# Kernel tuning notes

Measured on AMD Instinct MI355X. Metric: run time of the kernel, lower is better.

The kernel has to match this reference:

```python
import jax, jax.numpy as jnp
import numpy as np

B, C, IMG, PS, S, D, H, HD, L, OUT = 512, 3, 36, 6, 36, 768, 12, 64, 4, 256

def _pos_embedding(seq_len, dim):
    # NOTE: cos at even indices, sin at odd (as in the torch source)
    position = np.arange(seq_len, dtype=np.float32)[:, None]
    div = np.exp(np.arange(0, dim, 2, dtype=np.float32) * -(np.log(10000.0) / dim))
    emb = np.zeros((seq_len, dim), dtype=np.float32)
    emb[:, 0::2] = np.cos(position * div)
    emb[:, 1::2] = np.sin(position * div)
    return jnp.asarray(emb)

def setup_inputs():
    ks = jax.random.split(jax.random.key(0), 10)
    sc = lambda f: 1.0 / np.sqrt(f)
    return {
        'batch': jax.random.normal(ks[0], (B, C, IMG, IMG), jnp.float32),
        'W_patch': jax.random.normal(ks[1], (D, PS * PS), jnp.float32) * sc(PS * PS),
        'b_patch': jnp.zeros((D,), jnp.float32),
        'pos': _pos_embedding(S, D),
        'ln1_g': jnp.ones((L, D), jnp.float32),
        'ln1_b': jnp.zeros((L, D), jnp.float32),
        'Wq': jax.random.normal(ks[2], (L, H, HD, HD), jnp.float32) * sc(HD),
        'bq': jnp.zeros((L, H, HD), jnp.float32),
        'Wk': jax.random.normal(ks[3], (L, H, HD, HD), jnp.float32) * sc(HD),
        'bk': jnp.zeros((L, H, HD), jnp.float32),
        'Wv': jax.random.normal(ks[4], (L, H, HD, HD), jnp.float32) * sc(HD),
        'bv': jnp.zeros((L, H, HD), jnp.float32),
        'ln2_g': jnp.ones((L, D), jnp.float32),
        'ln2_b': jnp.zeros((L, D), jnp.float32),
        'W1': jax.random.normal(ks[5], (L, 2 * D, D), jnp.float32) * sc(D),
        'b1': jnp.zeros((L, 2 * D), jnp.float32),
        'W2': jax.random.normal(ks[6], (L, D, 2 * D), jnp.float32) * sc(2 * D),
        'b2': jnp.zeros((L, D), jnp.float32),
        'W_out': jax.random.normal(ks[7], (OUT, D), jnp.float32) * sc(D),
        'b_out': jnp.zeros((OUT,), jnp.float32),
    }

def _layernorm(x, g, b):
    m = jnp.mean(x, axis=-1, keepdims=True)
    v = jnp.mean((x - m) ** 2, axis=-1, keepdims=True)
    return (x - m) / jnp.sqrt(v + 1e-5) * g + b

def _forward(batch, W_patch, b_patch, pos, ln1_g, ln1_b, Wq, bq, Wk, bk, Wv, bv,
             ln2_g, ln2_b, W1, b1, W2, b2, W_out, b_out):
    b_, c_ = batch.shape[0], batch.shape[1]
    # patchify: (B,C,36,36) -> (B,C,36 patches,36 pixels), matching torch unfold+reshape
    p = batch.reshape(b_, c_, IMG // PS, PS, IMG // PS, PS)
    p = p.transpose(0, 1, 2, 4, 3, 5).reshape(b_, c_, S, PS * PS)
    z = p @ W_patch.T + b_patch + pos  # pos broadcasts over (B,C)
    scale = 1.0 / np.sqrt(HD)
    for l in range(L):
        # pre-LN then batched per-head attention (collapses the python loops)
        h = _layernorm(z, ln1_g[l], ln1_b[l]).reshape(b_, c_, S, H, HD)
        q = jnp.einsum('bcshd,hed->bcshe', h, Wq[l]) + bq[l]
        k = jnp.einsum('bcshd,hed->bcshe', h, Wk[l]) + bk[l]
        v = jnp.einsum('bcshd,hed->bcshe', h, Wv[l]) + bv[l]
        attn = jax.nn.softmax(jnp.einsum('bcshe,bcthe->bchst', q, k) * scale, axis=-1)
        o = jnp.einsum('bchst,bcthe->bcshe', attn, v).reshape(b_, c_, S, D)
        z = z + o
        z = _layernorm(z, ln2_g[l], ln2_b[l])
        z = z + (jax.nn.relu(z @ W1[l].T + b1[l]) @ W2[l].T + b2[l])
    return z @ W_out.T + b_out

def reference(batch, W_patch, b_patch, pos, ln1_g, ln1_b, Wq, bq, Wk, bk, Wv, bv,
              ln2_g, ln2_b, W1, b1, W2, b2, W_out, b_out):
    return _forward(batch, W_patch, b_patch, pos, ln1_g, ln1_b, Wq, bq, Wk, bk, Wv, bv,
                    ln2_g, ln2_b, W1, b1, W2, b2, W_out, b_out)
```

## Files before the change

### kernel.cpp

```cpp
#include <hip/hip_runtime.h>
#include <hip/hip_bf16.h>
#include <cstdint>
#include <cstddef>

typedef __bf16 bf16;
typedef bf16 bf16x8 __attribute__((ext_vector_type(8)));
typedef bf16 bf16x4 __attribute__((ext_vector_type(4)));
typedef float f32x4 __attribute__((ext_vector_type(4)));
typedef unsigned int u32;

#define GLD_LDS16(gptr, lptr)                                                        \
  __builtin_amdgcn_global_load_lds((const __attribute__((address_space(1))) u32*)(gptr), \
                                   (__attribute__((address_space(3))) u32*)(lptr), 16, 0, 0)

static constexpr int S = 36, D = 768, H = 12, HD = 64, DFF = 1536;
static constexpr int BC = 1536;
static constexpr int M = BC * S;
static constexpr int OUTD = 256;

__global__ __launch_bounds__(256) void f2b_kernel(const float* __restrict__ in,
                                                  bf16* __restrict__ out, int n4) {
  int i = blockIdx.x * 256 + threadIdx.x;
  if (i < n4) {
    float4 f = ((const float4*)in)[i];
    bf16x4 o = {(bf16)f.x, (bf16)f.y, (bf16)f.z, (bf16)f.w};
    ((bf16x4*)out)[i] = o;
  }
}

__global__ __launch_bounds__(256) void zerok(float* __restrict__ p, int n) {
  int i = blockIdx.x * 256 + threadIdx.x;
  if (i < n) p[i] = 0.f;
}
__global__ __launch_bounds__(256) void stats_fin(const float* __restrict__ sacc,
                                                 float* __restrict__ stats, int n) {
  int i = blockIdx.x * 256 + threadIdx.x;
  if (i < n) {
    float sm = sacc[(size_t)i * 2] * (1.f / 768.f);
    float sq = sacc[(size_t)i * 2 + 1] * (1.f / 768.f);
    float var = sq - sm * sm;
    stats[(size_t)i * 2] = sm;
    stats[(size_t)i * 2 + 1] = rsqrtf(var + 1e-5f);
  }
}

__global__ __launch_bounds__(64) void qk_prep(const float* __restrict__ Wq,
                                              const float* __restrict__ Wk,
                                              const float* __restrict__ bq,
                                              bf16* __restrict__ wb,
                                              float* __restrict__ vkout) {
  int lh = blockIdx.x;
  int e = threadIdx.x;
  __shared__ float Wqs[64][64];
  __shared__ float Wks[64][64];
  const float* wqp = Wq + (size_t)lh * 4096;
  const float* wkp = Wk + (size_t)lh * 4096;
  for (int i = e; i < 4096; i += 64) {
    Wqs[i >> 6][i & 63] = wqp[i];
    Wks[i >> 6][i & 63] = wkp[i];
  }
  __syncthreads();
  float ks[64];
#pragma unroll
  for (int f = 0; f < 64; ++f) ks[f] = Wks[f][e];
  for (int d0 = 0; d0 < 64; d0 += 4) {
    float a0 = 0.f, a1 = 0.f, a2 = 0.f, a3 = 0.f;
#pragma unroll
    for (int f = 0; f < 64; ++f) {
      float4 wq4 = *(const float4*)&Wqs[f][d0];
      a0 += wq4.x * ks[f]; a1 += wq4.y * ks[f];
      a2 += wq4.z * ks[f]; a3 += wq4.w * ks[f];
    }
    bf16x4 o = {(bf16)a0, (bf16)a1, (bf16)a2, (bf16)a3};
    *(bf16x4*)&wb[(size_t)lh * 4096 + e * 64 + d0] = o;
  }
  const float* bqp = bq + lh * 64;
  float acc = 0.f;
#pragma unroll
  for (int f = 0; f < 64; ++f) acc += ks[f] * bqp[f];
  vkout[lh * 64 + e] = acc;
}

__global__ __launch_bounds__(256) void patch_embed(const float* __restrict__ batch,
                                                   const float* __restrict__ Wp,
                                                   const float* __restrict__ bp,
                                                   const float* __restrict__ pos,
                                                   float* __restrict__ z) {
  int bc = blockIdx.x, tid = threadIdx.x;
  __shared__ float p[36][40];
  for (int i = tid; i < 1296; i += 256) {
    float f = batch[(size_t)bc * 1296 + i];
    int row = i / 36, col = i - row * 36;
    p[(row / 6) * 6 + col / 6][(row % 6) * 6 + (col % 6)] = f;
  }
  __syncthreads();
  for (int c0 = 0; c0 < 768; c0 += 256) {
    int d = c0 + tid;
    float wr[36];
    const float4* wp4 = (const float4*)(Wp + (size_t)d * 36);
#pragma unroll
    for (int q = 0; q < 9; ++q) {
      float4 f = wp4[q];
      wr[q * 4] = f.x; wr[q * 4 + 1] = f.y; wr[q * 4 + 2] = f.z; wr[q * 4 + 3] = f.w;
    }
    float gb = bp[d];
    for (int s = 0; s < 36; ++s) {
      float acc = 0.f;
#pragma unroll
      for (int k = 0; k < 36; ++k) acc += p[s][k] * wr[k];
      z[((size_t)bc * 36 + s) * 768 + d] = acc + gb + pos[s * 768 + d];
    }
  }
}

__global__ __launch_bounds__(256) void ln_stats(const float* __restrict__ zin,
                                                float* __restrict__ stats) {
  int row = blockIdx.x * 4 + (threadIdx.x >> 6);
  int lane = threadIdx.x & 63;
  const float* zr = zin + (size_t)row * D;
  float x[12];
#pragma unroll
  for (int i = 0; i < 12; ++i) x[i] = zr[i * 64 + lane];
  float s = 0.f;
#pragma unroll
  for (int i = 0; i < 12; ++i) s += x[i];
#pragma unroll
  for (int off = 32; off >= 1; off >>= 1) s += __shfl_xor(s, off, 64);
  float m = s * (1.f / 768.f);
  float v = 0.f;
#pragma unroll
  for (int i = 0; i < 12; ++i) { float dd = x[i] - m; v += dd * dd; }
#pragma unroll
  for (int off = 32; off >= 1; off >>= 1) v += __shfl_xor(v, off, 64);
  v *= (1.f / 768.f);
  if (lane == 0) {
    stats[(size_t)row * 2] = m;
    stats[(size_t)row * 2 + 1] = rsqrtf(v + 1e-5f);
  }
}

__global__ __launch_bounds__(256) void ln_inplace(float* __restrict__ z,
                                                  const float* __restrict__ g,
                                                  const float* __restrict__ bt) {
  int row = blockIdx.x * 4 + (threadIdx.x >> 6);
  int lane = threadIdx.x & 63;
  float* zr = z + (size_t)row * D;
  float x[12];
#pragma unroll
  for (int i = 0; i < 12; ++i) x[i] = zr[i * 64 + lane];
  float s = 0.f;
#pragma unroll
  for (int i = 0; i < 12; ++i) s += x[i];
#pragma unroll
  for (int off = 32; off >= 1; off >>= 1) s += __shfl_xor(s, off, 64);
  float m = s * (1.f / 768.f);
  float v = 0.f;
#pragma unroll
  for (int i = 0; i < 12; ++i) { float dd = x[i] - m; v += dd * dd; }
#pragma unroll
  for (int off = 32; off >= 1; off >>= 1) v += __shfl_xor(v, off, 64);
  v *= (1.f / 768.f);
  float rstd = rsqrtf(v + 1e-5f);
#pragma unroll
  for (int i = 0; i < 12; ++i) {
    int d = i * 64 + lane;
    zr[d] = (x[i] - m) * rstd * g[d] + bt[d];
  }
}

__global__ __launch_bounds__(64) void attn_kernel(const float* __restrict__ zg,
                                                  const float* __restrict__ stats,
                                                  const float* __restrict__ g1,
                                                  const float* __restrict__ b1_,
                                                  const bf16* __restrict__ Wqk,
                                                  const bf16* __restrict__ Wv,
                                                  const float* __restrict__ vk,
                                                  const float* __restrict__ bv,
                                                  float* __restrict__ z) {
  int head = blockIdx.x;
  int bc = blockIdx.y;
  __shared__ __align__(16) bf16 gb[48 * 72];
  __shared__ __align__(16) bf16 vt[64 * 72];
  int lane = threadIdx.x;
  int lr = lane & 15, quad = lane >> 4;

#pragma unroll
  for (int t0 = 0; t0 < 16; ++t0) vt[lane * 72 + 48 + t0] = (bf16)0.f;

  const float* zsrc = zg + ((size_t)bc * S) * D + head * HD;
  const float* st = stats + (size_t)bc * S * 2;

  float gv[2][8], bvv[2][8];
#pragma unroll
  for (int kt = 0; kt < 2; ++kt) {
    int c0 = head * HD + kt * 32 + quad * 8;
    float4 ga = *(const float4*)(g1 + c0);
    float4 gb2 = *(const float4*)(g1 + c0 + 4);
    float4 ba = *(const float4*)(b1_ + c0);
    float4 bb2 = *(const float4*)(b1_ + c0 + 4);
    gv[kt][0] = ga.x; gv[kt][1] = ga.y; gv[kt][2] = ga.z; gv[kt][3] = ga.w;
    gv[kt][4] = gb2.x; gv[kt][5] = gb2.y; gv[kt][6] = gb2.z; gv[kt][7] = gb2.w;
    bvv[kt][0] = ba.x; bvv[kt][1] = ba.y; bvv[kt][2] = ba.z; bvv[kt][3] = ba.w;
    bvv[kt][4] = bb2.x; bvv[kt][5] = bb2.y; bvv[kt][6] = bb2.z; bvv[kt][7] = bb2.w;
  }

  bf16x8 hfrag[3][2];
#pragma unroll
  for (int mt = 0; mt < 3; ++mt) {
    int srow = mt * 16 + lr;
    if (srow < 36) {
      float mm = st[srow * 2], rr = st[srow * 2 + 1];
#pragma unroll
      for (int kt = 0; kt < 2; ++kt) {
        int c0 = kt * 32 + quad * 8;
        float4 f0 = *(const float4*)(zsrc + (size_t)srow * D + c0);
        float4 f1 = *(const float4*)(zsrc + (size_t)srow * D + c0 + 4);
        float hv[8] = {f0.x, f0.y, f0.z, f0.w, f1.x, f1.y, f1.z, f1.w};
        bf16x8 o;
#pragma unroll
        for (int j = 0; j < 8; ++j) o[j] = (bf16)((hv[j] - mm) * rr * gv[kt][j] + bvv[kt][j]);
        hfrag[mt][kt] = o;
      }
    } else {
#pragma unroll
      for (int kt = 0; kt < 2; ++kt) {
        bf16x8 o;
#pragma unroll
        for (int j = 0; j < 8; ++j) o[j] = (bf16)0.f;
        hfrag[mt][kt] = o;
      }
    }
  }

  float vkv[2][8];
#pragma unroll
  for (int kt = 0; kt < 2; ++kt) {
    int c0 = head * 64 + kt * 32 + quad * 8;
    float4 va = *(const float4*)(vk + c0);
    float4 vb2 = *(const float4*)(vk + c0 + 4);
    vkv[kt][0] = va.x; vkv[kt][1] = va.y; vkv[kt][2] = va.z; vkv[kt][3] = va.w;
    vkv[kt][4] = vb2.x; vkv[kt][5] = vb2.y; vkv[kt][6] = vb2.z; vkv[kt][7] = vb2.w;
  }
  float tv[3];
#pragma unroll
  for (int mt = 0; mt < 3; ++mt) {
    float sp = 0.f;
#pragma unroll
    for (int kt = 0; kt < 2; ++kt)
#pragma unroll
      for (int j = 0; j < 8; ++j) sp += (float)hfrag[mt][kt][j] * vkv[kt][j];
    sp += __shfl_xor(sp, 16, 64);
    sp += __shfl_xor(sp, 32, 64);
    tv[mt] = sp;
  }

  const bf16* Wm[2] = {Wqk + (size_t)head * 4096, Wv + (size_t)head * 4096};
  const float* bvp = bv + head * 64;
  for (int p = 0; p < 2; ++p) {
    bf16x8 bfr[4][2];
#pragma unroll
    for (int nt = 0; nt < 4; ++nt)
#pragma unroll
      for (int kt = 0; kt < 2; ++kt)
        bfr[nt][kt] = *(const bf16x8*)(Wm[p] + (nt * 16 + lr) * 64 + kt * 32 + quad * 8);
#pragma unroll
    for (int mt = 0; mt < 3; ++mt) {
      f32x4 acc[4] = {};
#pragma unroll
      for (int kt = 0; kt < 2; ++kt)
#pragma unroll
        for (int nt = 0; nt < 4; ++nt)
          acc[nt] = __builtin_amdgcn_mfma_f32_16x16x32_bf16(hfrag[mt][kt], bfr[nt][kt], acc[nt], 0, 0, 0);
#pragma unroll
      for (int nt = 0; nt < 4; ++nt) {
        float bb = (p == 1) ? bvp[nt * 16 + lr] : 0.f;
#pragma unroll
        for (int r = 0; r < 4; ++r) {
          int s2 = mt * 16 + quad * 4 + r;
          int e = nt * 16 + lr;
          float val = acc[nt][r] + bb;
          if (p == 0) gb[s2 * 72 + e] = (bf16)val;
          else vt[e * 72 + s2] = (bf16)val;
        }
      }
    }
  }
  __syncthreads();

  f32x4 sc[3][3];
#pragma unroll
  for (int mt = 0; mt < 3; ++mt)
#pragma unroll
    for (int nt = 0; nt < 3; ++nt) {
      f32x4 a = {};
#pragma unroll
      for (int kt = 0; kt < 2; ++kt) {
        bf16x8 af = *(const bf16x8*)&gb[(mt * 16 + lr) * 72 + kt * 32 + quad * 8];
        a = __builtin_amdgcn_mfma_f32_16x16x32_bf16(af, hfrag[nt][kt], a, 0, 0, 0);
      }
      int t = nt * 16 + lr;
#pragma unroll
      for (int r = 0; r < 4; ++r) {
        float v = (a[r] + tv[nt]) * 0.125f;
        if (t >= 36) v = -1e30f;
        sc[mt][nt][r] = v;
      }
    }
  __syncthreads();

#pragma unroll
  for (int mt = 0; mt < 3; ++mt) {
    float mx[4], sum[4];
#pragma unroll
    for (int r = 0; r < 4; ++r)
      mx[r] = fmaxf(fmaxf(sc[mt][0][r], sc[mt][1][r]), sc[mt][2][r]);
#pragma unroll
    for (int r = 0; r < 4; ++r)
#pragma unroll
      for (int off = 8; off >= 1; off >>= 1) mx[r] = fmaxf(mx[r], __shfl_xor(mx[r], off, 64));
#pragma unroll
    for (int r = 0; r < 4; ++r) sum[r] = 0.f;
#pragma unroll
    for (int nt = 0; nt < 3; ++nt)
#pragma unroll
      for (int r = 0; r < 4; ++r) {
        float e = __expf(sc[mt][nt][r] - mx[r]);
        sc[mt][nt][r] = e;
        sum[r] += e;
      }
#pragma unroll
    for (int r = 0; r < 4; ++r)
#pragma unroll
      for (int off = 8; off >= 1; off >>= 1) sum[r] += __shfl_xor(sum[r], off, 64);
#pragma unroll
    for (int nt = 0; nt < 4; ++nt)
#pragma unroll
      for (int r = 0; r < 4; ++r) {
        int s2 = mt * 16 + quad * 4 + r;
        int t = nt * 16 + lr;
        float pv = (nt < 3) ? sc[mt][nt][r] / sum[r] : 0.f;
        gb[s2 * 72 + t] = (bf16)pv;
      }
  }
  __syncthreads();

#pragma unroll
  for (int mt = 0; mt < 3; ++mt) {
    f32x4 o[4] = {};
#pragma unroll
    for (int kt = 0; kt < 2; ++kt) {
      bf16x8 a = *(const bf16x8*)&gb[(mt * 16 + lr) * 72 + kt * 32 + quad * 8];
#pragma unroll
      for (int nt = 0; nt < 4; ++nt) {
        bf16x8 b = *(const bf16x8*)&vt[(nt * 16 + lr) * 72 + kt * 32 + quad * 8];
        o[nt] = __builtin_amdgcn_mfma_f32_16x16x32_bf16(a, b, o[nt], 0, 0, 0);
      }
    }
#pragma unroll
    for (int nt = 0; nt < 4; ++nt)
#pragma unroll
      for (int r = 0; r < 4; ++r) {
        int s2 = mt * 16 + quad * 4 + r;
        if (s2 < 36) {
          int e = nt * 16 + lr;
          size_t idx = ((size_t)bc * S + s2) * D + head * HD + e;
          z[idx] += o[nt][r];
        }
      }
  }
}

template <int N, int K, int MODE, int AF32>
__global__ __launch_bounds__(256) void gemm_bt(const void* __restrict__ A,
                                               const bf16* __restrict__ Bw,
                                               const float* __restrict__ bias,
                                               const float* __restrict__ res,
                                               void* __restrict__ outp,
                                               float* __restrict__ sacc) {
  constexpr int BK = 64;
  __shared__ __align__(16) bf16 As[128 * BK];
  __shared__ __align__(16) bf16 Bs[128 * BK];
  int tid = threadIdx.x;
  int bn = blockIdx.x, bm = blockIdx.y;
  if ((gridDim.y & 7) == 0) {
    int gx = gridDim.x, gy = gridDim.y;
    int h = bm * gx + bn;
    int x = h & 7, k = h >> 3;
    int gpc = gy >> 3;
    bm = x * gpc + k / gx;
    bn = k - (k / gx) * gx;
  }
  const bf16* Abf = (const bf16*)A + (size_t)bm * 128 * K;
  const float* Af = (const float*)A + (size_t)bm * 128 * K;
  const bf16* Bb = Bw + (size_t)bn * 128 * K;
  int lane = tid & 63, wave = tid >> 6;
  int wm = (wave >> 1) * 64, wn = (wave & 1) * 64;
  int lr = lane & 15, quad = lane >> 4;
  f32x4 acc[4][4] = {};
  for (int k0 = 0; k0 < K; k0 += BK) {
    if (AF32) {
#pragma unroll
      for (int r = 0; r < 8; ++r) {
        int c = r * 256 + tid;
        int row = c >> 4, col4 = (c & 15) * 4;
        float4 f = *(const float4*)(Af + (size_t)row * K + k0 + col4);
        bf16x4 o = {(bf16)f.x, (bf16)f.y, (bf16)f.z, (bf16)f.w};
        *(bf16x4*)&As[row * BK + col4] = o;
      }
    } else {
#pragma unroll
      for (int r = 0; r < 4; ++r) {
        int c = r * 256 + tid;
        int row = c >> 3, col = (c & 7) * 8;
        GLD_LDS16(Abf + (size_t)row * K + k0 + col, &As[c * 8]);
      }
    }
#pragma unroll
    for (int r = 0; r < 4; ++r) {
      int c = r * 256 + tid;
      int row = c >> 3, col = (c & 7) * 8;
      GLD_LDS16(Bb + (size_t)row * K + k0 + col, &Bs[c * 8]);
    }
    __syncthreads();
#pragma unroll
    for (int kt = 0; kt < 2; ++kt) {
      bf16x8 af[4], bfr[4];
#pragma unroll
      for (int mt = 0; mt < 4; ++mt) af[mt] = *(const bf16x8*)&As[(wm + mt * 16 + lr) * BK + kt * 32 + quad * 8];
#pragma unroll
      for (int nt = 0; nt < 4; ++nt) bfr[nt] = *(const bf16x8*)&Bs[(wn + nt * 16 + lr) * BK + kt * 32 + quad * 8];
#pragma unroll
      for (int mt = 0; mt < 4; ++mt)
#pragma unroll
        for (int nt = 0; nt < 4; ++nt)
          acc[mt][nt] = __builtin_amdgcn_mfma_f32_16x16x32_bf16(af[mt], bfr[nt], acc[mt][nt], 0, 0, 0);
    }
    __syncthreads();
  }
  int row0 = bm * 128 + wm + quad * 4;
  int col0 = bn * 128 + wn + lr;
  if (MODE == 4) {
#pragma unroll
    for (int mt = 0; mt < 4; ++mt)
#pragma unroll
      for (int r = 0; r < 4; ++r) {
        int row = row0 + mt * 16 + r;
        float rs = 0.f, rq = 0.f;
#pragma unroll
        for (int nt = 0; nt < 4; ++nt) {
          int col = col0 + nt * 16;
          size_t idx = (size_t)row * N + col;
          float o = acc[mt][nt][r] + bias[col] + res[idx];
          ((float*)outp)[idx] = o;
          rs += o; rq += o * o;
        }
#pragma unroll
        for (int off = 8; off >= 1; off >>= 1) {
          rs += __shfl_xor(rs, off, 64);
          rq += __shfl_xor(rq, off, 64);
        }
        if (lr == 0) {
          atomicAdd(&sacc[(size_t)row * 2], rs);
          atomicAdd(&sacc[(size_t)row * 2 + 1], rq);
        }
      }
  } else {
#pragma unroll
    for (int mt = 0; mt < 4; ++mt)
#pragma unroll
      for (int nt = 0; nt < 4; ++nt) {
        int col = col0 + nt * 16;
        float bv = bias[col];
#pragma unroll
        for (int r = 0; r < 4; ++r) {
          size_t idx = (size_t)(row0 + mt * 16 + r) * N + col;
          float v = acc[mt][nt][r] + bv;
          if (MODE == 0) ((bf16*)outp)[idx] = (bf16)fmaxf(v, 0.f);
          else if (MODE == 1) ((float*)outp)[idx] = v + res[idx];
          else ((float*)outp)[idx] = v;
        }
      }
  }
}

extern "C" void kernel_launch(void* const* d_in, const int* in_sizes, int n_in,
                              void* d_out, int out_size, void* d_ws, size_t ws_size,
                              hipStream_t stream) {
  const float* batch   = (const float*)d_in[0];
  const float* W_patch = (const float*)d_in[1];
  const float* b_patch = (const float*)d_in[2];
  const float* pos     = (const float*)d_in[3];
  const float* ln1_g   = (const float*)d_in[4];
  const float* ln1_b   = (const float*)d_in[5];
  const float* Wq      = (const float*)d_in[6];
  const float* bq      = (const float*)d_in[7];
  const float* Wk      = (const float*)d_in[8];
  const float* bk      = (const float*)d_in[9];
  const float* Wv      = (const float*)d_in[10];
  const float* bv      = (const float*)d_in[11];
  const float* ln2_g   = (const float*)d_in[12];
  const float* ln2_b   = (const float*)d_in[13];
  const float* W1      = (const float*)d_in[14];
  const float* b1      = (const float*)d_in[15];
  const float* W2      = (const float*)d_in[16];
  const float* b2      = (const float*)d_in[17];
  const float* W_out   = (const float*)d_in[18];
  const float* b_out   = (const float*)d_in[19];
  float* out = (float*)d_out;
  (void)bk;

  char* ws = (char*)d_ws;
  size_t off = 0;
  float* z     = (float*)(ws + off); off += (size_t)M * D * 4;
  float* stats = (float*)(ws + off); off += (size_t)M * 2 * 4;
  float* sacc  = (float*)(ws + off); off += (size_t)M * 2 * 4;
  bf16* wqk_b = (bf16*)(ws + off);   off += (size_t)4 * H * 4096 * 2;
  bf16* wv_b = (bf16*)(ws + off);    off += (size_t)4 * H * 4096 * 2;
  float* vk_f = (float*)(ws + off);  off += (size_t)4 * H * 64 * 4;
  bf16* w1_b = (bf16*)(ws + off);    off += (size_t)4 * DFF * D * 2;
  bf16* w2_b = (bf16*)(ws + off);    off += (size_t)4 * D * DFF * 2;
  bf16* wo_b = (bf16*)(ws + off);    off += (size_t)OUTD * D * 2;
  bf16* act  = (bf16*)(ws + off);

  size_t avail = ws_size > off ? ws_size - off : (size_t)0;
  long long rcl = (long long)(avail / ((size_t)DFF * 2));
  int rc = (rcl > (long long)M) ? M : (int)rcl;
  rc = (rc / 1024) * 1024;
  if (rc <= 0) rc = 128;

  qk_prep<<<48, 64, 0, stream>>>(Wq, Wk, bq, wqk_b, vk_f);
  f2b_kernel<<<192, 256, 0, stream>>>(Wv, wv_b, 49152);
  f2b_kernel<<<4608, 256, 0, stream>>>(W1, w1_b, 1179648);
  f2b_kernel<<<4608, 256, 0, stream>>>(W2, w2_b, 1179648);
  f2b_kernel<<<192, 256, 0, stream>>>(W_out, wo_b, 49152);

  patch_embed<<<BC, 256, 0, stream>>>(batch, W_patch, b_patch, pos, z);
  ln_stats<<<M / 4, 256, 0, stream>>>(z, stats);

  for (int l = 0; l < 4; ++l) {
    attn_kernel<<<dim3(H, BC), 64, 0, stream>>>(z, stats, ln1_g + l * D, ln1_b + l * D,
        wqk_b + (size_t)l * H * 4096, wv_b + (size_t)l * H * 4096,
        vk_f + (size_t)l * H * 64, bv + (size_t)l * H * 64, z);
    ln_inplace<<<M / 4, 256, 0, stream>>>(z, ln2_g + l * D, ln2_b + l * D);
    if (l < 3) zerok<<<(M * 2 + 255) / 256, 256, 0, stream>>>(sacc, M * 2);
    for (int m0 = 0; m0 < M; m0 += rc) {
      int mr = (M - m0 < rc) ? (M - m0) : rc;
      gemm_bt<DFF, D, 0, 1><<<dim3(DFF / 128, mr / 128), 256, 0, stream>>>(
          z + (size_t)m0 * D, w1_b + (size_t)l * DFF * D, b1 + l * DFF, nullptr, act, nullptr);
      if (l < 3)
        gemm_bt<D, DFF, 4, 0><<<dim3(D / 128, mr / 128), 256, 0, stream>>>(
            act, w2_b + (size_t)l * D * DFF, b2 + l * D, z + (size_t)m0 * D,
            z + (size_t)m0 * D, sacc + (size_t)m0 * 2);
      else
        gemm_bt<D, DFF, 1, 0><<<dim3(D / 128, mr / 128), 256, 0, stream>>>(
            act, w2_b + (size_t)l * D * DFF, b2 + l * D, z + (size_t)m0 * D,
            z + (size_t)m0 * D, nullptr);
    }
    if (l < 3) stats_fin<<<(M + 255) / 256, 256, 0, stream>>>(sacc, stats, M);
  }

  gemm_bt<OUTD, D, 2, 1><<<dim3(OUTD / 128, M / 128), 256, 0, stream>>>(
      z, wo_b, b_out, nullptr, out, nullptr);
}
```

Baseline: 3.395 ms.

## Use 256x256 double-buffered MLP GEMMs with bf16 LN output per row chunk

Adds a 512-thread GEMM kernel with 256x256 tiles, BK=32 and two LDS buffers filled by async global-to-LDS loads, and uses it for both MLP GEMMs in place of the 128x128 single-buffered kernel. The LN2 kernel now also writes a bf16 copy of its output and runs per row chunk, so the first GEMM reads bf16 directly instead of converting fp32 on load. The goals are more data reuse per tile, overlap of loads with MFMA, and less A-operand traffic. The costs are extra workspace for the bf16 copy, higher register and LDS pressure from the larger tile, and coarser row-chunk granularity.

```diff
diff --git a/kernel.cpp b/kernel.cpp
--- a/kernel.cpp
+++ b/kernel.cpp
@@ -141,7 +141,8 @@
 
 __global__ __launch_bounds__(256) void ln_inplace(float* __restrict__ z,
                                                   const float* __restrict__ g,
-                                                  const float* __restrict__ bt) {
+                                                  const float* __restrict__ bt,
+                                                  bf16* __restrict__ zb) {
   int row = blockIdx.x * 4 + (threadIdx.x >> 6);
   int lane = threadIdx.x & 63;
   float* zr = z + (size_t)row * D;
@@ -161,10 +162,13 @@
   for (int off = 32; off >= 1; off >>= 1) v += __shfl_xor(v, off, 64);
   v *= (1.f / 768.f);
   float rstd = rsqrtf(v + 1e-5f);
+  bf16* zbr = zb ? zb + (size_t)row * D : nullptr;
 #pragma unroll
   for (int i = 0; i < 12; ++i) {
     int d = i * 64 + lane;
-    zr[d] = (x[i] - m) * rstd * g[d] + bt[d];
+    float o = (x[i] - m) * rstd * g[d] + bt[d];
+    zr[d] = o;
+    if (zbr) zbr[d] = (bf16)o;
   }
 }
 
@@ -370,13 +374,131 @@
   }
 }
 
+template <int N, int K, int MODE>
+__global__ __launch_bounds__(512) void gemm256(const bf16* __restrict__ A,
+                                               const bf16* __restrict__ Bw,
+                                               const float* __restrict__ bias,
+                                               const float* __restrict__ res,
+                                               void* __restrict__ outp,
+                                               float* __restrict__ sacc) {
+  constexpr int BK = 32;
+  constexpr int T = K / BK;
+  __shared__ __align__(16) bf16 As[2][256 * BK];
+  __shared__ __align__(16) bf16 Bs[2][256 * BK];
+  int tid = threadIdx.x;
+  int bn = blockIdx.x, bm = blockIdx.y;
+  if ((gridDim.y & 7) == 0) {
+    int gx = gridDim.x, gy = gridDim.y;
+    int h = bm * gx + bn;
+    int x = h & 7, k = h >> 3;
+    int gpc = gy >> 3;
+    bm = x * gpc + k / gx;
+    bn = k - (k / gx) * gx;
+  }
+  const bf16* Ab = A + (size_t)bm * 256 * K;
+  const bf16* Bb = Bw + (size_t)bn * 256 * K;
+  int lane = tid & 63, wave = tid >> 6;
+  int wm = wave >> 2, wn = wave & 3;
+  int lr = lane & 15, quad = lane >> 4;
+
+  auto stage = [&](int slot, int t) {
+    int k0 = t * BK;
+#pragma unroll
+    for (int r = 0; r < 2; ++r) {
+      int u = r * 512 + tid;
+      int row = u >> 2, col = (u & 3) * 8;
+      GLD_LDS16(Ab + (size_t)row * K + k0 + col, &As[slot][u * 8]);
+    }
+#pragma unroll
+    for (int r = 0; r < 2; ++r) {
+      int u = r * 512 + tid;
+      int row = u >> 2, col = (u & 3) * 8;
+      GLD_LDS16(Bb + (size_t)row * K + k0 + col, &Bs[slot][u * 8]);
+    }
+  };
+
+  f32x4 acc[8][4] = {};
+  stage(0, 0);
+  stage(1, 1);
+  asm volatile("s_waitcnt vmcnt(4)" ::: "memory");
+  __builtin_amdgcn_s_barrier();
+  __builtin_amdgcn_sched_barrier(0);
+
+  for (int t = 0; t < T; ++t) {
+    int s = t & 1;
+    bf16x8 bfr[4];
+#pragma unroll
+    for (int nt = 0; nt < 4; ++nt)
+      bfr[nt] = *(const bf16x8*)&Bs[s][(wn * 64 + nt * 16 + lr) * BK + quad * 8];
+#pragma unroll
+    for (int mt = 0; mt < 8; ++mt) {
+      bf16x8 af = *(const bf16x8*)&As[s][(wm * 128 + mt * 16 + lr) * BK + quad * 8];
+#pragma unroll
+      for (int nt = 0; nt < 4; ++nt)
+        acc[mt][nt] = __builtin_amdgcn_mfma_f32_16x16x32_bf16(af, bfr[nt], acc[mt][nt], 0, 0, 0);
+    }
+    __builtin_amdgcn_sched_barrier(0);
+    __builtin_amdgcn_s_barrier();
+    if (t + 2 < T) stage(s, t + 2);
+    if (t + 1 < T) {
+      if (t + 2 < T) asm volatile("s_waitcnt vmcnt(4)" ::: "memory");
+      else           asm volatile("s_waitcnt vmcnt(0)" ::: "memory");
+      __builtin_amdgcn_s_barrier();
+      __builtin_amdgcn_sched_barrier(0);
+    }
+  }
+
+  int row0 = bm * 256 + wm * 128 + quad * 4;
+  int col0 = bn * 256 + wn * 64 + lr;
+  if (MODE == 4) {
+#pragma unroll
+    for (int mt = 0; mt < 8; ++mt)
+#pragma unroll
+      for (int r = 0; r < 4; ++r) {
+        int row = row0 + mt * 16 + r;
+        float rs = 0.f, rq = 0.f;
+#pragma unroll
+        for (int nt = 0; nt < 4; ++nt) {
+          int col = col0 + nt * 16;
+          size_t idx = (size_t)row * N + col;
+          float o = acc[mt][nt][r] + bias[col] + res[idx];
+          ((float*)outp)[idx] = o;
+          rs += o; rq += o * o;
+        }
+#pragma unroll
+        for (int off = 8; off >= 1; off >>= 1) {
+          rs += __shfl_xor(rs, off, 64);
+          rq += __shfl_xor(rq, off, 64);
+        }
+        if (lr == 0) {
+          atomicAdd(&sacc[(size_t)row * 2], rs);
+          atomicAdd(&sacc[(size_t)row * 2 + 1], rq);
+        }
+      }
+  } else {
+#pragma unroll
+    for (int mt = 0; mt < 8; ++mt)
+#pragma unroll
+      for (int nt = 0; nt < 4; ++nt) {
+        int col = col0 + nt * 16;
+        float bv = bias[col];
+#pragma unroll
+        for (int r = 0; r < 4; ++r) {
+          size_t idx = (size_t)(row0 + mt * 16 + r) * N + col;
+          float v = acc[mt][nt][r] + bv;
+          if (MODE == 0) ((bf16*)outp)[idx] = (bf16)fmaxf(v, 0.f);
+          else ((float*)outp)[idx] = v + res[idx];
+        }
+      }
+  }
+}
+
 template <int N, int K, int MODE, int AF32>
 __global__ __launch_bounds__(256) void gemm_bt(const void* __restrict__ A,
                                                const bf16* __restrict__ Bw,
                                                const float* __restrict__ bias,
                                                const float* __restrict__ res,
-                                               void* __restrict__ outp,
-                                               float* __restrict__ sacc) {
+                                               void* __restrict__ outp) {
   constexpr int BK = 64;
   __shared__ __align__(16) bf16 As[128 * BK];
   __shared__ __align__(16) bf16 Bs[128 * BK];
@@ -439,48 +561,21 @@
   }
   int row0 = bm * 128 + wm + quad * 4;
   int col0 = bn * 128 + wn + lr;
-  if (MODE == 4) {
-#pragma unroll
-    for (int mt = 0; mt < 4; ++mt)
+#pragma unroll
+  for (int mt = 0; mt < 4; ++mt)
+#pragma unroll
+    for (int nt = 0; nt < 4; ++nt) {
+      int col = col0 + nt * 16;
+      float bv = bias[col];
 #pragma unroll
       for (int r = 0; r < 4; ++r) {
-        int row = row0 + mt * 16 + r;
-        float rs = 0.f, rq = 0.f;
-#pragma unroll
-        for (int nt = 0; nt < 4; ++nt) {
-          int col = col0 + nt * 16;
-          size_t idx = (size_t)row * N + col;
-          float o = acc[mt][nt][r] + bias[col] + res[idx];
-          ((float*)outp)[idx] = o;
-          rs += o; rq += o * o;
-        }
-#pragma unroll
-        for (int off = 8; off >= 1; off >>= 1) {
-          rs += __shfl_xor(rs, off, 64);
-          rq += __shfl_xor(rq, off, 64);
-        }
-        if (lr == 0) {
-          atomicAdd(&sacc[(size_t)row * 2], rs);
-          atomicAdd(&sacc[(size_t)row * 2 + 1], rq);
-        }
-      }
-  } else {
-#pragma unroll
-    for (int mt = 0; mt < 4; ++mt)
-#pragma unroll
-      for (int nt = 0; nt < 4; ++nt) {
-        int col = col0 + nt * 16;
-        float bv = bias[col];
-#pragma unroll
-        for (int r = 0; r < 4; ++r) {
-          size_t idx = (size_t)(row0 + mt * 16 + r) * N + col;
-          float v = acc[mt][nt][r] + bv;
-          if (MODE == 0) ((bf16*)outp)[idx] = (bf16)fmaxf(v, 0.f);
-          else if (MODE == 1) ((float*)outp)[idx] = v + res[idx];
-          else ((float*)outp)[idx] = v;
-        }
-      }
-  }
+        size_t idx = (size_t)(row0 + mt * 16 + r) * N + col;
+        float v = acc[mt][nt][r] + bv;
+        if (MODE == 0) ((bf16*)outp)[idx] = (bf16)fmaxf(v, 0.f);
+        else if (MODE == 1) ((float*)outp)[idx] = v + res[idx];
+        else ((float*)outp)[idx] = v;
+      }
+    }
 }
 
 extern "C" void kernel_launch(void* const* d_in, const int* in_sizes, int n_in,
@@ -520,13 +615,14 @@
   bf16* w1_b = (bf16*)(ws + off);    off += (size_t)4 * DFF * D * 2;
   bf16* w2_b = (bf16*)(ws + off);    off += (size_t)4 * D * DFF * 2;
   bf16* wo_b = (bf16*)(ws + off);    off += (size_t)OUTD * D * 2;
-  bf16* act  = (bf16*)(ws + off);
 
   size_t avail = ws_size > off ? ws_size - off : (size_t)0;
-  long long rcl = (long long)(avail / ((size_t)DFF * 2));
+  long long rcl = (long long)(avail / ((size_t)(DFF + D) * 2));
   int rc = (rcl > (long long)M) ? M : (int)rcl;
-  rc = (rc / 1024) * 1024;
-  if (rc <= 0) rc = 128;
+  rc = (rc / 2048) * 2048;
+  if (rc <= 0) rc = 2048;
+  bf16* act = (bf16*)(ws + off);  off += (size_t)rc * DFF * 2;
+  bf16* zbc = (bf16*)(ws + off);
 
   qk_prep<<<48, 64, 0, stream>>>(Wq, Wk, bq, wqk_b, vk_f);
   f2b_kernel<<<192, 256, 0, stream>>>(Wv, wv_b, 49152);
@@ -541,18 +637,19 @@
     attn_kernel<<<dim3(H, BC), 64, 0, stream>>>(z, stats, ln1_g + l * D, ln1_b + l * D,
         wqk_b + (size_t)l * H * 4096, wv_b + (size_t)l * H * 4096,
         vk_f + (size_t)l * H * 64, bv + (size_t)l * H * 64, z);
-    ln_inplace<<<M / 4, 256, 0, stream>>>(z, ln2_g + l * D, ln2_b + l * D);
     if (l < 3) zerok<<<(M * 2 + 255) / 256, 256, 0, stream>>>(sacc, M * 2);
     for (int m0 = 0; m0 < M; m0 += rc) {
       int mr = (M - m0 < rc) ? (M - m0) : rc;
-      gemm_bt<DFF, D, 0, 1><<<dim3(DFF / 128, mr / 128), 256, 0, stream>>>(
-          z + (size_t)m0 * D, w1_b + (size_t)l * DFF * D, b1 + l * DFF, nullptr, act, nullptr);
+      ln_inplace<<<mr / 4, 256, 0, stream>>>(z + (size_t)m0 * D, ln2_g + l * D,
+                                             ln2_b + l * D, zbc);
+      gemm256<DFF, D, 0><<<dim3(DFF / 256, mr / 256), 512, 0, stream>>>(
+          zbc, w1_b + (size_t)l * DFF * D, b1 + l * DFF, nullptr, act, nullptr);
       if (l < 3)
-        gemm_bt<D, DFF, 4, 0><<<dim3(D / 128, mr / 128), 256, 0, stream>>>(
+        gemm256<D, DFF, 4><<<dim3(D / 256, mr / 256), 512, 0, stream>>>(
             act, w2_b + (size_t)l * D * DFF, b2 + l * D, z + (size_t)m0 * D,
             z + (size_t)m0 * D, sacc + (size_t)m0 * 2);
       else
-        gemm_bt<D, DFF, 1, 0><<<dim3(D / 128, mr / 128), 256, 0, stream>>>(
+        gemm256<D, DFF, 1><<<dim3(D / 256, mr / 256), 512, 0, stream>>>(
             act, w2_b + (size_t)l * D * DFF, b2 + l * D, z + (size_t)m0 * D,
             z + (size_t)m0 * D, nullptr);
     }
@@ -560,5 +657,5 @@
   }
 
   gemm_bt<OUTD, D, 2, 1><<<dim3(OUTD / 128, M / 128), 256, 0, stream>>>(
-      z, wo_b, b_out, nullptr, out, nullptr);
-}
+      z, wo_b, b_out, nullptr, out);
+}
```

After: 3.609 ms. 1.06x slower.
